# Optimization experiments

Hardware: AMD Instinct MI355X
Metric: run time of the kernel (lower is better)

## Reference

```python
import jax, jax.numpy as jnp
import numpy as np


def _sparse_mask(T, S, W, G):
    """Replicates CustomSparseAttention._create_sparse_mask (bool [T, S])."""
    ii = np.arange(T)[:, None]
    jj = np.arange(S)[None, :]
    # local sliding window: cols in [i - W//2, i + W//2]
    m = (jj >= ii - W // 2) & (jj <= ii + W // 2)
    # overlapping block windows every (W - W//4) rows
    ov = W // 4
    for i in range(0, T, W - ov):
        m[i:i + W, max(0, i - ov):min(S, i + W + ov)] = True
    # strided global tokens
    if G > 0:
        stride = S // (G + 1)
        gi = np.linspace(stride, S - stride, G).astype(np.int64)  # torch .long() truncates
        m[:, gi] = True
    # diagonal +/- 1
    m |= np.abs(jj - ii) <= 1
    return jnp.asarray(m)


def setup_inputs() -> dict:
    key = jax.random.key(0)
    ks = jax.random.split(key, 8)
    B, T, S, E = 2, 2048, 2048, 512
    std = 0.02
    return {
        "query": jax.random.normal(ks[0], (B, T, E), jnp.float32),
        "key": jax.random.normal(ks[1], (B, S, E), jnp.float32),
        "value": jax.random.normal(ks[2], (B, S, E), jnp.float32),
        "Wq": jax.random.normal(ks[3], (E, E), jnp.float32) * std,
        "bq": jnp.zeros((E,), jnp.float32),
        "Wk": jax.random.normal(ks[4], (E, E), jnp.float32) * std,
        "bk": jnp.zeros((E,), jnp.float32),
        "Wv": jax.random.normal(ks[5], (E, E), jnp.float32) * std,
        "bv": jnp.zeros((E,), jnp.float32),
        "Wo": jax.random.normal(ks[6], (E, E), jnp.float32) * std,
        "bo": jnp.zeros((E,), jnp.float32),
        "temperature": jnp.ones((1,), jnp.float32) * 0.1,
        "local_window_size": 128,
        "num_global_tokens": 16,
    }


def reference(query, key, value, Wq, bq, Wk, bk, Wv, bv, Wo, bo,
              temperature, local_window_size, num_global_tokens):
    B, T, E = query.shape
    S = key.shape[1]
    H = 16
    hd = E // H
    scaling = float(hd) ** -0.5

    q = (query @ Wq.T + bq) * scaling          # [B, T, E]
    k = key @ Wk.T + bk                        # [B, S, E]
    v = value @ Wv.T + bv                      # [B, S, E]

    q = q.reshape(B, T, H, hd)
    k = k.reshape(B, S, H, hd)
    v = v.reshape(B, S, H, hd)

    # [B, H, T, S] dense scores, scaled by learned temperature
    attn = jnp.einsum('bthd,bshd->bhts', q, k) * temperature[0]

    mask = _sparse_mask(T, S, local_window_size, num_global_tokens)  # [T, S] bool
    attn = jnp.where(mask[None, None], attn, -jnp.inf)

    # (row-max subtraction in the original is the standard stable softmax)
    attn = jax.nn.softmax(attn, axis=-1)

    out = jnp.einsum('bhts,bshd->bthd', attn, v).reshape(B, T, E)
    out = out @ Wo.T + bo
    return out
```

## Files before the change

kernel.cpp:

```cpp
#include <hip/hip_runtime.h>

typedef _Float16 f16x8 __attribute__((ext_vector_type(8)));
typedef float f32x4 __attribute__((ext_vector_type(4)));

#define Tt 2048
#define Ee 512
#define Hh 16
#define HD 32
#define Bb 2
#define Mm (Bb*Tt)

__device__ __constant__ int GCOLS[16] = {120,240,361,481,602,722,843,963,
                                         1084,1204,1325,1445,1566,1686,1807,1928};

__device__ __forceinline__ int lo_of(int i) {
    int kmin = (i >= 32) ? ((i - 32) / 96) : 0;
    int lo = kmin * 96 - 32;
    return lo < 0 ? 0 : lo;
}
__device__ __forceinline__ int hi_of(int i) {
    int hi = (i / 96) * 96 + 160;
    return hi > Tt ? Tt : hi;
}

__device__ __forceinline__ f16x8 cvt8(float4 a, float4 b) {
    f16x8 r;
    r[0]=(_Float16)a.x; r[1]=(_Float16)a.y; r[2]=(_Float16)a.z; r[3]=(_Float16)a.w;
    r[4]=(_Float16)b.x; r[5]=(_Float16)b.y; r[6]=(_Float16)b.z; r[7]=(_Float16)b.w;
    return r;
}

__device__ __forceinline__ void async_copy16(const _Float16* g, _Float16* l) {
    __builtin_amdgcn_global_load_lds(
        (const __attribute__((address_space(1))) void*)g,
        (__attribute__((address_space(3))) void*)l, 16, 0, 0);
}

__global__ __launch_bounds__(256)
void proj_kernel(const float* __restrict__ qx, const float* __restrict__ kx,
                 const float* __restrict__ vx,
                 const float* __restrict__ Wq, const float* __restrict__ Wk,
                 const float* __restrict__ Wv, const float* __restrict__ Wo,
                 const float* __restrict__ bq, const float* __restrict__ bk,
                 const float* __restrict__ bv, const float* __restrict__ temp,
                 _Float16* __restrict__ q_ws, _Float16* __restrict__ k_ws,
                 _Float16* __restrict__ v_ws, _Float16* __restrict__ wof)
{
    const int z = blockIdx.z;
    const float* A = (z == 0) ? qx : (z == 1) ? kx : vx;
    const float* W = (z == 0) ? Wq : (z == 1) ? Wk : Wv;
    const float* bias = (z == 0) ? bq : (z == 1) ? bk : bv;

    {
        const int fb = blockIdx.x + 64 * blockIdx.y + 256 * blockIdx.z;
        if (fb < 128) {
            const int g8 = fb * 256 + threadIdx.x;
            const float* src = Wo + (size_t)g8 * 8;
            float4 a = ((const float4*)src)[0];
            float4 b = ((const float4*)src)[1];
            *(f16x8*)(wof + (size_t)g8 * 8) = cvt8(a, b);
        }
    }

    const int m0 = blockIdx.x * 64;
    const int n0 = blockIdx.y * 128;

    __shared__ _Float16 Ash[64 * 64];
    __shared__ _Float16 Bsh[128 * 64];

    const int tid  = threadIdx.x;
    const int lane = tid & 63, wave = tid >> 6;
    const int quad = lane >> 4, l16 = lane & 15;
    const int wm = wave & 1, wn = wave >> 1;

    const int sl = lane >> 3;
    const int lcol = ((lane & 7) ^ sl) * 8;
    const float* aS[2] = {
        A + (size_t)(m0 + wave*8      + sl) * Ee + lcol,
        A + (size_t)(m0 + (4+wave)*8  + sl) * Ee + lcol };
    const float* bS[4] = {
        W + (size_t)(n0 + wave*8      + sl) * Ee + lcol,
        W + (size_t)(n0 + (4+wave)*8  + sl) * Ee + lcol,
        W + (size_t)(n0 + (8+wave)*8  + sl) * Ee + lcol,
        W + (size_t)(n0 + (12+wave)*8 + sl) * Ee + lcol };
    _Float16* aD[2] = { Ash + wave*512 + lane*8, Ash + (4+wave)*512 + lane*8 };
    _Float16* bD[4] = { Bsh + wave*512 + lane*8, Bsh + (4+wave)*512 + lane*8,
                        Bsh + (8+wave)*512 + lane*8, Bsh + (12+wave)*512 + lane*8 };

    float4 pa[2][2][2];
    float4 pb[2][4][2];

    #pragma unroll
    for (int u = 0; u < 2; ++u) {
        pa[0][u][0] = ((const float4*)(aS[u]))[0];
        pa[0][u][1] = ((const float4*)(aS[u]))[1];
    }
    #pragma unroll
    for (int u = 0; u < 4; ++u) {
        pb[0][u][0] = ((const float4*)(bS[u]))[0];
        pb[0][u][1] = ((const float4*)(bS[u]))[1];
    }

    f32x4 acc[2][4] = {};

    #pragma unroll
    for (int it = 0; it < 8; ++it) {
        const int cur = it & 1, nxt = cur ^ 1;

        __syncthreads();
        #pragma unroll
        for (int u = 0; u < 2; ++u)
            *(f16x8*)aD[u] = cvt8(pa[cur][u][0], pa[cur][u][1]);
        #pragma unroll
        for (int u = 0; u < 4; ++u)
            *(f16x8*)bD[u] = cvt8(pb[cur][u][0], pb[cur][u][1]);

        if (it < 7) {
            const int k0 = (it + 1) * 64;
            #pragma unroll
            for (int u = 0; u < 2; ++u) {
                pa[nxt][u][0] = ((const float4*)(aS[u] + k0))[0];
                pa[nxt][u][1] = ((const float4*)(aS[u] + k0))[1];
            }
            #pragma unroll
            for (int u = 0; u < 4; ++u) {
                pb[nxt][u][0] = ((const float4*)(bS[u] + k0))[0];
                pb[nxt][u][1] = ((const float4*)(bS[u] + k0))[1];
            }
        }
        __syncthreads();

        #pragma unroll
        for (int kk = 0; kk < 2; kk++) {
            f16x8 af[2], bf[4];
            #pragma unroll
            for (int mt = 0; mt < 2; mt++) {
                const int row = wm*32 + mt*16 + l16;
                af[mt] = *(const f16x8*)&Ash[row*64 + (((kk*4+quad) ^ (row & 7)) * 8)];
            }
            #pragma unroll
            for (int nt = 0; nt < 4; nt++) {
                const int row = wn*64 + nt*16 + l16;
                bf[nt] = *(const f16x8*)&Bsh[row*64 + (((kk*4+quad) ^ (row & 7)) * 8)];
            }
            #pragma unroll
            for (int mt = 0; mt < 2; mt++)
                #pragma unroll
                for (int nt = 0; nt < 4; nt++)
                    acc[mt][nt] = __builtin_amdgcn_mfma_f32_16x16x32_f16(af[mt], bf[nt], acc[mt][nt], 0, 0, 0);
        }
    }

    const float scale = (z == 0) ? (0.17677669529663687f * temp[0]) : 1.0f;
    #pragma unroll
    for (int nt = 0; nt < 4; nt++) {
        const int n = n0 + wn * 64 + nt * 16 + l16;
        const float bn = bias[n];
        const int h = n >> 5, d = n & 31;
        #pragma unroll
        for (int mt = 0; mt < 2; mt++) {
            #pragma unroll
            for (int r = 0; r < 4; r++) {
                const int m = m0 + wm * 32 + mt * 16 + quad * 4 + r;
                const float val = (acc[mt][nt][r] + bn) * scale;
                const int bidx = m >> 11, t = m & (Tt - 1);
                if (z == 2) {
                    v_ws[((size_t)(bidx * Hh + h) * HD + d) * Tt + t] = (_Float16)val;
                } else {
                    _Float16* dst = (z == 0) ? q_ws : k_ws;
                    dst[((size_t)(bidx * Hh + h) * Tt + t) * HD + d] = (_Float16)val;
                }
            }
        }
    }
}

__global__ __launch_bounds__(256)
void attn_kernel(const _Float16* __restrict__ q_ws, const _Float16* __restrict__ k_ws,
                 const _Float16* __restrict__ v_ws, _Float16* __restrict__ o_ws)
{
    const int linear = blockIdx.x;
    const int xcd = linear & 7;
    const int p   = linear >> 3;
    const int bh  = xcd + 8 * (p & 3);
    const int qb  = (p >> 2) * 64;
    const int h   = bh & 15;
    const int b   = bh >> 4;

    const int tid  = threadIdx.x;
    const int lane = tid & 63, wave = tid >> 6;
    const int quad = lane >> 4, l16 = lane & 15;
    const int t0   = qb + wave * 16;

    __shared__ _Float16 P_lds[4][16*72];
    _Float16* myP = &P_lds[wave][0];

    const f16x8 qf = *(const f16x8*)(q_ws + ((size_t)bh*Tt + t0 + l16)*HD + quad*8);

    int lo[4], len[4];
    #pragma unroll
    for (int r = 0; r < 4; r++) {
        const int i = t0 + quad*4 + r;
        lo[r] = lo_of(i); len[r] = hi_of(i) - lo[r];
    }

    float lsum[4] = {0.f, 0.f, 0.f, 0.f};
    f32x4 accO[2] = {};
    const f32x4 zf = {0.f, 0.f, 0.f, 0.f};

    const int cstart = lo_of(t0) & ~63;
    const int cend   = hi_of(t0 + 15);

    f16x8 kcur[4];
    #pragma unroll
    for (int nt = 0; nt < 4; nt++)
        kcur[nt] = *(const f16x8*)(k_ws + ((size_t)bh*Tt + cstart + nt*16 + l16)*HD + quad*8);

    {
        const int gj = GCOLS[l16];
        const f16x8 kg = *(const f16x8*)(k_ws + ((size_t)bh*Tt + gj)*HD + quad*8);
        const f32x4 s = __builtin_amdgcn_mfma_f32_16x16x32_f16(qf, kg, zf, 0, 0, 0);
        #pragma unroll
        for (int r = 0; r < 4; r++) {
            const bool inside = (unsigned)(gj - lo[r]) < (unsigned)len[r];
            const float p2 = inside ? 0.f : __expf(s[r]);
            const _Float16 ph = (_Float16)p2;
            lsum[r] += (float)ph;
            myP[(quad*4 + r)*72 + l16] = ph;
        }
        f16x8 pf;
        if (quad < 2) pf = *(const f16x8*)&myP[l16*72 + quad*8];
        else {
            #pragma unroll
            for (int j = 0; j < 8; j++) pf[j] = (_Float16)0.f;
        }
        int gck[8];
        #pragma unroll
        for (int j = 0; j < 8; j++) gck[j] = (quad < 2) ? GCOLS[quad*8 + j] : 0;
        #pragma unroll
        for (int dt = 0; dt < 2; dt++) {
            f16x8 vg;
            if (quad < 2) {
                const _Float16* vrow = v_ws + ((size_t)bh*HD + dt*16 + l16)*Tt;
                #pragma unroll
                for (int j = 0; j < 8; j++) vg[j] = vrow[gck[j]];
            } else {
                #pragma unroll
                for (int j = 0; j < 8; j++) vg[j] = (_Float16)0.f;
            }
            accO[dt] = __builtin_amdgcn_mfma_f32_16x16x32_f16(pf, vg, accO[dt], 0, 0, 0);
        }
    }

    for (int j0 = cstart; j0 < cend; j0 += 64) {
        f16x8 knxt[4];
        const int jn = j0 + 64;
        if (jn < cend) {
            #pragma unroll
            for (int nt = 0; nt < 4; nt++)
                knxt[nt] = *(const f16x8*)(k_ws + ((size_t)bh*Tt + jn + nt*16 + l16)*HD + quad*8);
        }

        f32x4 s[4];
        #pragma unroll
        for (int nt = 0; nt < 4; nt++)
            s[nt] = __builtin_amdgcn_mfma_f32_16x16x32_f16(qf, kcur[nt], zf, 0, 0, 0);
        #pragma unroll
        for (int nt = 0; nt < 4; nt++) {
            const int j = j0 + nt*16 + l16;
            #pragma unroll
            for (int r = 0; r < 4; r++) {
                const bool inside = (unsigned)(j - lo[r]) < (unsigned)len[r];
                const float p2 = inside ? __expf(s[nt][r]) : 0.f;
                const _Float16 ph = (_Float16)p2;
                lsum[r] += (float)ph;
                myP[(quad*4 + r)*72 + nt*16 + l16] = ph;
            }
        }
        #pragma unroll
        for (int kt = 0; kt < 2; kt++) {
            const f16x8 pf = *(const f16x8*)&myP[l16*72 + kt*32 + quad*8];
            #pragma unroll
            for (int dt = 0; dt < 2; dt++) {
                const f16x8 vf = *(const f16x8*)(v_ws + ((size_t)bh*HD + dt*16 + l16)*Tt
                                                 + j0 + kt*32 + quad*8);
                accO[dt] = __builtin_amdgcn_mfma_f32_16x16x32_f16(pf, vf, accO[dt], 0, 0, 0);
            }
        }

        #pragma unroll
        for (int nt = 0; nt < 4; nt++) kcur[nt] = knxt[nt];
    }

    #pragma unroll
    for (int r = 0; r < 4; r++) {
        float v = lsum[r];
        v += __shfl_xor(v, 1);
        v += __shfl_xor(v, 2);
        v += __shfl_xor(v, 4);
        v += __shfl_xor(v, 8);
        lsum[r] = 1.0f / v;
    }
    #pragma unroll
    for (int dt = 0; dt < 2; dt++) {
        #pragma unroll
        for (int r = 0; r < 4; r++) {
            const int t = t0 + quad*4 + r;
            const int d = dt*16 + l16;
            o_ws[((size_t)(b*Tt + t)*Hh + h)*HD + d] = (_Float16)(accO[dt][r] * lsum[r]);
        }
    }
}

__global__ __launch_bounds__(256)
void out_kernel(const _Float16* __restrict__ Aw, const _Float16* __restrict__ Wof,
                const float* __restrict__ bo, float* __restrict__ out)
{
    const int m0 = blockIdx.x * 64;
    const int n0 = blockIdx.y * 128;

    __shared__ _Float16 Ash[64 * 64];
    __shared__ _Float16 Bsh[128 * 64];

    const int tid  = threadIdx.x;
    const int lane = tid & 63, wave = tid >> 6;
    const int quad = lane >> 4, l16 = lane & 15;
    const int wm = wave & 1, wn = wave >> 1;

    const int sl = lane >> 3;
    const int lcol = ((lane & 7) ^ sl) * 8;
    const _Float16* aSrc0 = Aw  + (size_t)(m0 + wave*8      + sl) * Ee + lcol;
    const _Float16* aSrc1 = Aw  + (size_t)(m0 + (4+wave)*8  + sl) * Ee + lcol;
    const _Float16* bSrc0 = Wof + (size_t)(n0 + wave*8      + sl) * Ee + lcol;
    const _Float16* bSrc1 = Wof + (size_t)(n0 + (4+wave)*8  + sl) * Ee + lcol;
    const _Float16* bSrc2 = Wof + (size_t)(n0 + (8+wave)*8  + sl) * Ee + lcol;
    const _Float16* bSrc3 = Wof + (size_t)(n0 + (12+wave)*8 + sl) * Ee + lcol;

    f32x4 acc[2][4] = {};

    for (int k0 = 0; k0 < Ee; k0 += 64) {
        __syncthreads();
        async_copy16(aSrc0 + k0, Ash + wave*512);
        async_copy16(aSrc1 + k0, Ash + (4+wave)*512);
        async_copy16(bSrc0 + k0, Bsh + wave*512);
        async_copy16(bSrc1 + k0, Bsh + (4+wave)*512);
        async_copy16(bSrc2 + k0, Bsh + (8+wave)*512);
        async_copy16(bSrc3 + k0, Bsh + (12+wave)*512);
        __syncthreads();

        #pragma unroll
        for (int kk = 0; kk < 2; kk++) {
            f16x8 af[2], bf[4];
            #pragma unroll
            for (int mt = 0; mt < 2; mt++) {
                const int row = wm*32 + mt*16 + l16;
                af[mt] = *(const f16x8*)&Ash[row*64 + (((kk*4+quad) ^ (row & 7)) * 8)];
            }
            #pragma unroll
            for (int nt = 0; nt < 4; nt++) {
                const int row = wn*64 + nt*16 + l16;
                bf[nt] = *(const f16x8*)&Bsh[row*64 + (((kk*4+quad) ^ (row & 7)) * 8)];
            }
            #pragma unroll
            for (int mt = 0; mt < 2; mt++)
                #pragma unroll
                for (int nt = 0; nt < 4; nt++)
                    acc[mt][nt] = __builtin_amdgcn_mfma_f32_16x16x32_f16(af[mt], bf[nt], acc[mt][nt], 0, 0, 0);
        }
    }

    #pragma unroll
    for (int nt = 0; nt < 4; nt++) {
        const int n = n0 + wn * 64 + nt * 16 + l16;
        const float bn = bo[n];
        #pragma unroll
        for (int mt = 0; mt < 2; mt++) {
            #pragma unroll
            for (int r = 0; r < 4; r++) {
                const int m = m0 + wm * 32 + mt * 16 + quad * 4 + r;
                out[(size_t)m * Ee + n] = acc[mt][nt][r] + bn;
            }
        }
    }
}

extern "C" void kernel_launch(void* const* d_in, const int* in_sizes, int n_in,
                              void* d_out, int out_size, void* d_ws, size_t ws_size,
                              hipStream_t stream)
{
    const float* query = (const float*)d_in[0];
    const float* key_  = (const float*)d_in[1];
    const float* value = (const float*)d_in[2];
    const float* Wq    = (const float*)d_in[3];
    const float* bq    = (const float*)d_in[4];
    const float* Wk    = (const float*)d_in[5];
    const float* bk    = (const float*)d_in[6];
    const float* Wv    = (const float*)d_in[7];
    const float* bv    = (const float*)d_in[8];
    const float* Wo    = (const float*)d_in[9];
    const float* bo    = (const float*)d_in[10];
    const float* temp  = (const float*)d_in[11];

    _Float16* xw   = (_Float16*)d_ws;
    _Float16* q_ws = xw + 7340032;
    _Float16* k_ws = q_ws + (size_t)Mm * Ee;
    _Float16* v_ws = k_ws + (size_t)Mm * Ee;
    _Float16* o_ws = v_ws + (size_t)Mm * Ee;
    _Float16* wof  = xw + (size_t)3 * Mm * Ee + (size_t)3 * Ee * Ee;
    float* out = (float*)d_out;

    proj_kernel<<<dim3(64, 4, 3), 256, 0, stream>>>(query, key_, value,
                                                    Wq, Wk, Wv, Wo,
                                                    bq, bk, bv, temp,
                                                    q_ws, k_ws, v_ws, wof);
    attn_kernel<<<dim3(1024), 256, 0, stream>>>(q_ws, k_ws, v_ws, o_ws);
    out_kernel<<<dim3(64, 4), 256, 0, stream>>>(o_ws, wof, bo, out);
}
```

Baseline: 140.7 us.

## Software-pipeline attention loop with double-buffered P tiles in LDS

Restructures the per-wave attention loop so the QK^T scores and exp for the next 64-column chunk are computed while the PV MMAs of the current chunk run. The P tile is double-buffered in LDS, and the V loads and P reads for the current chunk are issued at the top of the iteration. This is meant to hide global-load and LDS latency across the two MFMA phases. In exchange it doubles the P LDS footprint and adds register pressure from holding V fragments and the next scores at the same time.

```diff
diff --git a/kernel.cpp b/kernel.cpp
--- a/kernel.cpp
+++ b/kernel.cpp
@@ -192,8 +192,8 @@
     const int quad = lane >> 4, l16 = lane & 15;
     const int t0   = qb + wave * 16;
 
-    __shared__ _Float16 P_lds[4][16*72];
-    _Float16* myP = &P_lds[wave][0];
+    __shared__ _Float16 P_lds[4][2][16*72];
+    _Float16* bufP[2] = { &P_lds[wave][0][0], &P_lds[wave][1][0] };
 
     const f16x8 qf = *(const f16x8*)(q_ws + ((size_t)bh*Tt + t0 + l16)*HD + quad*8);
 
@@ -211,14 +211,18 @@
     const int cstart = lo_of(t0) & ~63;
     const int cend   = hi_of(t0 + 15);
 
+    const _Float16* kbase = k_ws + (size_t)bh*Tt*HD;
+    const _Float16* vbase = v_ws + (size_t)bh*HD*Tt;
+
     f16x8 kcur[4];
     #pragma unroll
     for (int nt = 0; nt < 4; nt++)
-        kcur[nt] = *(const f16x8*)(k_ws + ((size_t)bh*Tt + cstart + nt*16 + l16)*HD + quad*8);
+        kcur[nt] = *(const f16x8*)(kbase + (size_t)(cstart + nt*16 + l16)*HD + quad*8);
 
     {
+        _Float16* myP = bufP[0];
         const int gj = GCOLS[l16];
-        const f16x8 kg = *(const f16x8*)(k_ws + ((size_t)bh*Tt + gj)*HD + quad*8);
+        const f16x8 kg = *(const f16x8*)(kbase + (size_t)gj*HD + quad*8);
         const f32x4 s = __builtin_amdgcn_mfma_f32_16x16x32_f16(qf, kg, zf, 0, 0, 0);
         #pragma unroll
         for (int r = 0; r < 4; r++) {
@@ -241,7 +245,7 @@
         for (int dt = 0; dt < 2; dt++) {
             f16x8 vg;
             if (quad < 2) {
-                const _Float16* vrow = v_ws + ((size_t)bh*HD + dt*16 + l16)*Tt;
+                const _Float16* vrow = vbase + (size_t)(dt*16 + l16)*Tt;
                 #pragma unroll
                 for (int j = 0; j < 8; j++) vg[j] = vrow[gck[j]];
             } else {
@@ -252,44 +256,72 @@
         }
     }
 
-    for (int j0 = cstart; j0 < cend; j0 += 64) {
-        f16x8 knxt[4];
-        const int jn = j0 + 64;
-        if (jn < cend) {
-            #pragma unroll
-            for (int nt = 0; nt < 4; nt++)
-                knxt[nt] = *(const f16x8*)(k_ws + ((size_t)bh*Tt + jn + nt*16 + l16)*HD + quad*8);
-        }
-
+    {
         f32x4 s[4];
         #pragma unroll
         for (int nt = 0; nt < 4; nt++)
             s[nt] = __builtin_amdgcn_mfma_f32_16x16x32_f16(qf, kcur[nt], zf, 0, 0, 0);
+        if (cstart + 64 < cend) {
+            #pragma unroll
+            for (int nt = 0; nt < 4; nt++)
+                kcur[nt] = *(const f16x8*)(kbase + (size_t)(cstart + 64 + nt*16 + l16)*HD + quad*8);
+        }
         #pragma unroll
         for (int nt = 0; nt < 4; nt++) {
-            const int j = j0 + nt*16 + l16;
+            const int j = cstart + nt*16 + l16;
             #pragma unroll
             for (int r = 0; r < 4; r++) {
                 const bool inside = (unsigned)(j - lo[r]) < (unsigned)len[r];
                 const float p2 = inside ? __expf(s[nt][r]) : 0.f;
                 const _Float16 ph = (_Float16)p2;
                 lsum[r] += (float)ph;
-                myP[(quad*4 + r)*72 + nt*16 + l16] = ph;
-            }
-        }
-        #pragma unroll
-        for (int kt = 0; kt < 2; kt++) {
-            const f16x8 pf = *(const f16x8*)&myP[l16*72 + kt*32 + quad*8];
-            #pragma unroll
-            for (int dt = 0; dt < 2; dt++) {
-                const f16x8 vf = *(const f16x8*)(v_ws + ((size_t)bh*HD + dt*16 + l16)*Tt
-                                                 + j0 + kt*32 + quad*8);
-                accO[dt] = __builtin_amdgcn_mfma_f32_16x16x32_f16(pf, vf, accO[dt], 0, 0, 0);
-            }
-        }
-
-        #pragma unroll
-        for (int nt = 0; nt < 4; nt++) kcur[nt] = knxt[nt];
+                bufP[0][(quad*4 + r)*72 + nt*16 + l16] = ph;
+            }
+        }
+    }
+
+    int c = 0;
+    for (int j0 = cstart; j0 < cend; j0 += 64, c ^= 1) {
+        f16x8 pf0, pf1, vf[2][2];
+        pf0 = *(const f16x8*)&bufP[c][l16*72 + 0*32 + quad*8];
+        pf1 = *(const f16x8*)&bufP[c][l16*72 + 1*32 + quad*8];
+        #pragma unroll
+        for (int kt = 0; kt < 2; kt++)
+            #pragma unroll
+            for (int dt = 0; dt < 2; dt++)
+                vf[kt][dt] = *(const f16x8*)(vbase + (size_t)(dt*16 + l16)*Tt
+                                             + j0 + kt*32 + quad*8);
+
+        const int jn = j0 + 64;
+        if (jn < cend) {
+            f32x4 s[4];
+            #pragma unroll
+            for (int nt = 0; nt < 4; nt++)
+                s[nt] = __builtin_amdgcn_mfma_f32_16x16x32_f16(qf, kcur[nt], zf, 0, 0, 0);
+            if (jn + 64 < cend) {
+                #pragma unroll
+                for (int nt = 0; nt < 4; nt++)
+                    kcur[nt] = *(const f16x8*)(kbase + (size_t)(jn + 64 + nt*16 + l16)*HD + quad*8);
+            }
+            #pragma unroll
+            for (int nt = 0; nt < 4; nt++) {
+                const int j = jn + nt*16 + l16;
+                #pragma unroll
+                for (int r = 0; r < 4; r++) {
+                    const bool inside = (unsigned)(j - lo[r]) < (unsigned)len[r];
+                    const float p2 = inside ? __expf(s[nt][r]) : 0.f;
+                    const _Float16 ph = (_Float16)p2;
+                    lsum[r] += (float)ph;
+                    bufP[c ^ 1][(quad*4 + r)*72 + nt*16 + l16] = ph;
+                }
+            }
+        }
+
+        #pragma unroll
+        for (int dt = 0; dt < 2; dt++) {
+            accO[dt] = __builtin_amdgcn_mfma_f32_16x16x32_f16(pf0, vf[0][dt], accO[dt], 0, 0, 0);
+            accO[dt] = __builtin_amdgcn_mfma_f32_16x16x32_f16(pf1, vf[1][dt], accO[dt], 0, 0, 0);
+        }
     }
 
     #pragma unroll
```

Result: slower. 146.5 us (+4.1%).
